# Kernel optimization log

Measured on AMD Instinct MI355X. Metric: run time of the kernel, lower is better.

## Reference

```python
import jax, jax.numpy as jnp
import numpy as np

N_NODES = 50000
N_EDGES = 1600000
IN_DIM = 16
HID = 128
N_ITER = 3
EPS = 1e-8


def _rownorm(x):
    # x / (||x||_2 per row + 1e-8), matching torch.norm(p='fro', dim=1, keepdim=True)
    return x / (jnp.linalg.norm(x, axis=-1, keepdims=True) + EPS)


def setup_inputs() -> dict:
    key = jax.random.key(0)
    ks = jax.random.split(key, 16)
    s = 0.05  # small init scale for numerical sanity
    inp = {
        'feat': jax.random.normal(ks[0], (N_NODES, IN_DIM), dtype=jnp.float32),
        'src': jax.random.randint(ks[1], (N_EDGES,), 0, N_NODES, dtype=jnp.int32),
        'dst': jax.random.randint(ks[2], (N_EDGES,), 0, N_NODES, dtype=jnp.int32),
        'init_W0': jax.random.normal(ks[3], (IN_DIM, HID), dtype=jnp.float32) * s,
        'init_b0': jnp.zeros((HID,), dtype=jnp.float32),
        'init_W1': jax.random.normal(ks[4], (HID, HID), dtype=jnp.float32) * s,
        'init_b1': jnp.zeros((HID,), dtype=jnp.float32),
        'init_W2': jax.random.normal(ks[5], (HID, HID), dtype=jnp.float32) * s,
        'init_b2': jnp.zeros((HID,), dtype=jnp.float32),
        'node_W0': jax.random.normal(ks[6], (N_ITER, 3 * HID, HID), dtype=jnp.float32) * s,
        'node_b0': jnp.zeros((N_ITER, HID), dtype=jnp.float32),
        'node_W1': jax.random.normal(ks[7], (N_ITER, HID, HID), dtype=jnp.float32) * s,
        'node_b1': jnp.zeros((N_ITER, HID), dtype=jnp.float32),
        'node_W2': jax.random.normal(ks[8], (N_ITER, HID, HID), dtype=jnp.float32) * s,
        'node_b2': jnp.zeros((N_ITER, HID), dtype=jnp.float32),
    }
    return inp


def reference(feat, src, dst,
              init_W0, init_b0, init_W1, init_b1, init_W2, init_b2,
              node_W0, node_b0, node_W1, node_b1, node_W2, node_b2):
    n = feat.shape[0]

    # init_network: MLP (Linear+ReLU for hidden layers, linear output)
    h = jax.nn.relu(feat @ init_W0 + init_b0)
    h = jax.nn.relu(h @ init_W1 + init_b1)
    h = h @ init_W2 + init_b2  # [N, HID]

    # global representation: normalized sum over all nodes (single graph)
    gr = _rownorm(jnp.sum(h, axis=0, keepdims=True))  # [1, HID]

    # DGL update_all only updates nodes with >=1 incoming edge
    deg = jax.ops.segment_sum(jnp.ones_like(src, dtype=jnp.float32), dst,
                              num_segments=n)
    has_in = (deg > 0)[:, None]  # [N, 1]

    for i in range(node_W0.shape[0]):
        # copy_u + mailbox sum == gather src features, segment-sum by dst
        msg = jax.ops.segment_sum(h[src], dst, num_segments=n)  # [N, HID]
        inp = jnp.concatenate(
            [msg, h, jnp.broadcast_to(gr, (n, gr.shape[1]))], axis=1)  # [N, 3*HID]
        out = jax.nn.relu(inp @ node_W0[i] + node_b0[i])
        out = jax.nn.relu(out @ node_W1[i] + node_b1[i])
        out = out @ node_W2[i] + node_b2[i]
        out = _rownorm(out)
        h = jnp.where(has_in, out, h)
        gr = _rownorm(jnp.sum(h, axis=0, keepdims=True))

    return h
```

## Files before the change

kernel.cpp:

```cpp
#include <hip/hip_runtime.h>
#include <hip/hip_bf16.h>

#define HID 128
#define IN_DIM 16
#define LDST 136
#define NBSH 6
#define BPAD 16
#define SRCM 0x3ffffffu
#define CH 8192
#define NBMAX 1024
#define NDPW 4

typedef unsigned short u16;
typedef __attribute__((ext_vector_type(8))) short short8;
typedef __attribute__((ext_vector_type(4))) float f32x4;

__device__ __forceinline__ u16 f2b(float f) {
    unsigned u = __float_as_uint(f);
    return (u16)((u + 0x7FFF + ((u >> 16) & 1)) >> 16);
}


__global__ __launch_bounds__(256) void hist_k(const int* __restrict__ dst, int* __restrict__ bktcnt,
                                              int E, int nb) {
    __shared__ int hist[NBMAX];
    int tid = threadIdx.x;
    int base = blockIdx.x * CH;
    int cnt = E - base; if (cnt > CH) cnt = CH;
    for (int i = tid; i < nb; i += 256) hist[i] = 0;
    __syncthreads();
    for (int j = tid; j < cnt; j += 256) atomicAdd(&hist[dst[base + j] >> NBSH], 1);
    __syncthreads();
    for (int i = tid; i < nb; i += 256) {
        int c = hist[i];
        if (c > 0) atomicAdd(&bktcnt[i], c);
    }
}

__global__ __launch_bounds__(1024) void bscan_k(const int* __restrict__ bktcnt, int* __restrict__ bktbase,
                                                int* __restrict__ bcnt, int* __restrict__ row_ptr,
                                                int nb, int n, int E) {
    __shared__ int sbuf[1024];
    int t = threadIdx.x;
    int v = (t < nb) ? bktcnt[t] : 0;
    sbuf[t] = v;
    __syncthreads();
    for (int off = 1; off < 1024; off <<= 1) {
        int a = (t >= off) ? sbuf[t - off] : 0;
        __syncthreads();
        sbuf[t] += a;
        __syncthreads();
    }
    if (t < nb) {
        int excl = sbuf[t] - v;
        bktbase[t] = excl;
        bcnt[t * BPAD] = excl;
    }
    if (t == 0) { bktbase[nb] = E; row_ptr[n] = E; }
}

__global__ __launch_bounds__(256) void bin_k(const int* __restrict__ src, const int* __restrict__ dst,
                                             int* __restrict__ bcnt, unsigned* __restrict__ ebuf,
                                             int E, int nb) {
    __shared__ unsigned stage[CH];
    __shared__ u16 sbk[CH];
    __shared__ int hist[NBMAX];
    __shared__ int lofs[NBMAX];
    __shared__ int sbase[NBMAX];
    __shared__ int scan256[256];
    int tid = threadIdx.x;
    int base = blockIdx.x * CH;
    int cnt = E - base; if (cnt > CH) cnt = CH;

    for (int i = tid; i < nb; i += 256) hist[i] = 0;
    __syncthreads();
    for (int j = tid; j < cnt; j += 256) {
        int d = dst[base + j];
        atomicAdd(&hist[d >> NBSH], 1);
    }
    __syncthreads();
    int psum[4];
    int ts = 0;
#pragma unroll
    for (int q = 0; q < 4; q++) {
        int idx = tid * 4 + q;
        int hv = (idx < nb) ? hist[idx] : 0;
        psum[q] = ts;
        ts += hv;
    }
    scan256[tid] = ts;
    __syncthreads();
    for (int off = 1; off < 256; off <<= 1) {
        int a = (tid >= off) ? scan256[tid - off] : 0;
        __syncthreads();
        scan256[tid] += a;
        __syncthreads();
    }
    int tbase = (tid > 0) ? scan256[tid - 1] : 0;
#pragma unroll
    for (int q = 0; q < 4; q++) {
        int idx = tid * 4 + q;
        if (idx < nb) lofs[idx] = tbase + psum[q];
    }
    __syncthreads();
    for (int i = tid; i < nb; i += 256) {
        int c = hist[i];
        if (c > 0) {
            int g = atomicAdd(&bcnt[i * BPAD], c);
            sbase[i] = g - lofs[i];
        }
    }
    __syncthreads();
    for (int j = tid; j < cnt; j += 256) {
        int e = base + j;
        int d = dst[e];
        int b = d >> NBSH;
        int r = atomicAdd(&lofs[b], 1);
        stage[r] = (unsigned)src[e] | ((unsigned)(d & 63) << 26);
        sbk[r] = (u16)b;
    }
    __syncthreads();
    for (int s = tid; s < cnt; s += 256) {
        int b = sbk[s];
        ebuf[sbase[b] + s] = stage[s];
    }
}

__global__ __launch_bounds__(256) void fill2_k(const unsigned* __restrict__ ebuf, const int* __restrict__ bktbase,
                                               int* __restrict__ row_ptr, int* __restrict__ deg,
                                               int* __restrict__ srcs, int n) {
    __shared__ int hist64[64];
    __shared__ int lofs[64];
    int tid = threadIdx.x;
    int b = blockIdx.x;
    int e0 = bktbase[b], e1 = bktbase[b + 1];
    if (tid < 64) hist64[tid] = 0;
    __syncthreads();
    for (int i = e0 + tid; i < e1; i += 256) atomicAdd(&hist64[ebuf[i] >> 26], 1);
    __syncthreads();
    if (tid < 64) {
        int d = hist64[tid];
        int s = d;
#pragma unroll
        for (int off = 1; off < 64; off <<= 1) {
            int t = __shfl_up(s, off);
            if (tid >= off) s += t;
        }
        int excl = e0 + s - d;
        int gi = (b << NBSH) + tid;
        if (gi < n) { row_ptr[gi] = excl; deg[gi] = d; }
        lofs[tid] = excl;
    }
    __syncthreads();
    for (int i = e0 + tid; i < e1; i += 256) {
        unsigned p = ebuf[i];
        int d = (int)(p >> 26);
        int pos = atomicAdd(&lofs[d], 1);
        srcs[pos] = (int)(p & SRCM);
    }
}


struct WJobs {
    const float* src[16];
    int dstoff[16];
    int ks[16];
};

__global__ __launch_bounds__(256) void wprep_k(WJobs j, u16* __restrict__ Wt,
                                               int* __restrict__ bktcnt, float* __restrict__ gsums,
                                               int nb, int gz) {
    int m = blockIdx.x;
    if (m == 0) {
        for (int i = threadIdx.x; i < nb; i += 256) bktcnt[i] = 0;
    } else if (m == 1) {
        for (int i = threadIdx.x; i < gz; i += 256) gsums[i] = 0.f;
    }
    const float* s = j.src[m];
    u16* d = Wt + j.dstoff[m];
    int ks = j.ks[m];
    if (ks == 8) {
        for (int idx = threadIdx.x; idx < 16384; idx += 256) {
            int jj = idx & 7;
            int lane = (idx >> 3) & 63;
            int ni = (idx >> 9) & 3;
            int kk = (idx >> 11) & 3;
            int half = idx >> 13;
            int k = kk * 32 + (lane >> 4) * 8 + jj;
            int col = half * 64 + ni * 16 + (lane & 15);
            d[idx] = f2b(s[k * HID + col]);
        }
        return;
    }
    int K = 1 << ks;
    int tot = K * HID;
    for (int idx = threadIdx.x; idx < tot; idx += 256) {
        int nn = idx >> ks;
        int kk = idx & (K - 1);
        d[idx] = f2b(s[kk * HID + nn]);
    }
}


__device__ __forceinline__ void unpack_add(uint4 v, float* a) {
    a[0] += __uint_as_float(v.x << 16);
    a[1] += __uint_as_float(v.x & 0xffff0000u);
    a[2] += __uint_as_float(v.y << 16);
    a[3] += __uint_as_float(v.y & 0xffff0000u);
    a[4] += __uint_as_float(v.z << 16);
    a[5] += __uint_as_float(v.z & 0xffff0000u);
    a[6] += __uint_as_float(v.w << 16);
    a[7] += __uint_as_float(v.w & 0xffff0000u);
}

__global__ __launch_bounds__(256) void msg_k(const u16* __restrict__ hb, const int* __restrict__ row_ptr,
                                             const int* __restrict__ srcs, u16* __restrict__ msgb, int n,
                                             const float* __restrict__ gsumIn, const float* __restrict__ Wg,
                                             const float* __restrict__ b0, float* __restrict__ grW) {
    if (blockIdx.x == gridDim.x - 1) {
        __shared__ float sred[2];
        __shared__ float sgr[HID];
        int t = threadIdx.x;
        if (t < HID) {
            float g = gsumIn[t];
            float s = g * g;
#pragma unroll
            for (int off = 1; off < 64; off <<= 1) s += __shfl_xor(s, off);
            if ((t & 63) == 0) sred[t >> 6] = s;
        }
        __syncthreads();
        if (t < HID) {
            float inv = 1.f / (sqrtf(sred[0] + sred[1]) + 1e-8f);
            sgr[t] = gsumIn[t] * inv;
        }
        __syncthreads();
        if (t < HID) {
            float a = b0[t];
#pragma unroll 4
            for (int k = 0; k < HID; k++) a += sgr[k] * Wg[k * HID + t];
            grW[t] = a;
        }
        return;
    }
    int wave = threadIdx.x >> 6, lane = threadIdx.x & 63;
    int g = lane >> 4;
    int l16 = lane & 15;
    int d0 = (blockIdx.x * 4 + wave) * NDPW;
    if (d0 >= n) return;
    int eNext = row_ptr[d0];
#pragma unroll 1
    for (int k = 0; k < NDPW; k++) {
        int d = d0 + k;
        if (d >= n) break;
        int e = eNext;
        int e1 = row_ptr[d + 1];
        eNext = e1;
        float a[8] = {0.f, 0.f, 0.f, 0.f, 0.f, 0.f, 0.f, 0.f};
        int s0 = 0, s1 = 0, s2 = 0, s3 = 0;
        if (e + 15 < e1) {
            s0 = srcs[e + g]; s1 = srcs[e + 4 + g];
            s2 = srcs[e + 8 + g]; s3 = srcs[e + 12 + g];
        }
        while (e + 15 < e1) {
            int t0 = s0, t1 = s1, t2 = s2, t3 = s3;
            int en = e + 16;
            if (en + 15 < e1) {
                s0 = srcs[en + g]; s1 = srcs[en + 4 + g];
                s2 = srcs[en + 8 + g]; s3 = srcs[en + 12 + g];
            }
            uint4 v0 = *(const uint4*)(hb + (size_t)t0 * HID + l16 * 8);
            uint4 v1 = *(const uint4*)(hb + (size_t)t1 * HID + l16 * 8);
            uint4 v2 = *(const uint4*)(hb + (size_t)t2 * HID + l16 * 8);
            uint4 v3 = *(const uint4*)(hb + (size_t)t3 * HID + l16 * 8);
            unpack_add(v0, a);
            unpack_add(v1, a);
            unpack_add(v2, a);
            unpack_add(v3, a);
            e = en;
        }
        if (e + 7 < e1) {
            int t0 = srcs[e + g], t1 = srcs[e + 4 + g];
            uint4 v0 = *(const uint4*)(hb + (size_t)t0 * HID + l16 * 8);
            uint4 v1 = *(const uint4*)(hb + (size_t)t1 * HID + l16 * 8);
            unpack_add(v0, a);
            unpack_add(v1, a);
            e += 8;
        }
        if (e + 3 < e1) {
            int s = srcs[e + g];
            uint4 v = *(const uint4*)(hb + (size_t)s * HID + l16 * 8);
            unpack_add(v, a);
            e += 4;
        }
        if (e + g < e1) {
            int s = srcs[e + g];
            uint4 v = *(const uint4*)(hb + (size_t)s * HID + l16 * 8);
            unpack_add(v, a);
        }
#pragma unroll
        for (int i = 0; i < 8; i++) {
            a[i] += __shfl_xor(a[i], 16);
            a[i] += __shfl_xor(a[i], 32);
        }
        if (g == 0) {
            uint4 o;
            o.x = (unsigned)f2b(a[0]) | ((unsigned)f2b(a[1]) << 16);
            o.y = (unsigned)f2b(a[2]) | ((unsigned)f2b(a[3]) << 16);
            o.z = (unsigned)f2b(a[4]) | ((unsigned)f2b(a[5]) << 16);
            o.w = (unsigned)f2b(a[6]) | ((unsigned)f2b(a[7]) << 16);
            *(uint4*)(msgb + (size_t)d * HID + l16 * 8) = o;
        }
    }
}


__device__ __forceinline__ void load_tile(const u16* __restrict__ base, int tid, uint4 p[4]) {
#pragma unroll
    for (int q = 0; q < 4; q++) {
        int c = tid + q * 512;
        p[q] = *(const uint4*)(base + (size_t)(c >> 4) * HID + (c & 15) * 8);
    }
}

__device__ __forceinline__ void write_tile(const uint4 p[4], int tid, u16* s) {
#pragma unroll
    for (int q = 0; q < 4; q++) {
        int c = tid + q * 512;
        *(uint4*)(s + (c >> 4) * LDST + (c & 15) * 8) = p[q];
    }
}

__device__ __forceinline__ void load_tile64(const u16* __restrict__ base, int tid, uint4 p[4]) {
#pragma unroll
    for (int q = 0; q < 4; q++) {
        int c = tid + q * 256;
        p[q] = *(const uint4*)(base + (size_t)(c >> 4) * HID + (c & 15) * 8);
    }
}

__device__ __forceinline__ void write_tile64(const uint4 p[4], int tid, u16* s) {
#pragma unroll
    for (int q = 0; q < 4; q++) {
        int c = tid + q * 256;
        *(uint4*)(s + (c >> 4) * LDST + (c & 15) * 8) = p[q];
    }
}

__device__ __forceinline__ void stageFeat(const float* __restrict__ feat, int row0, int n, int tid, u16* sA) {
    int row = tid >> 2, coff = tid & 3;
    ushort4 o = make_ushort4(0, 0, 0, 0);
    if (row0 + row < n) {
        float4 v = *(const float4*)(feat + (size_t)(row0 + row) * IN_DIM + coff * 4);
        o = make_ushort4(f2b(v.x), f2b(v.y), f2b(v.z), f2b(v.w));
    }
    *(ushort4*)(sA + row * LDST + coff * 4) = o;
    *(ushort4*)(sA + row * LDST + 16 + coff * 4) = make_ushort4(0, 0, 0, 0);
}

__device__ __forceinline__ void stageW16(const u16* __restrict__ Wt, int tid, u16* sB) {
    if (tid < 256) {
        int row = tid >> 1, h8 = tid & 1;
        uint4 v = *(const uint4*)(Wt + row * IN_DIM + h8 * 8);
        *(uint4*)(sB + row * LDST + h8 * 8) = v;
        *(uint4*)(sB + row * LDST + 16 + h8 * 8) = make_uint4(0, 0, 0, 0);
    }
}

template <int KSTEPS>
__device__ __forceinline__ void mac(const u16* sA, const u16* sB, int wrow, int wcol,
                                    int ln15, int quad, f32x4 acc[2][4]) {
#pragma unroll
    for (int kk = 0; kk < KSTEPS; kk++) {
        short8 a[2], b[4];
#pragma unroll
        for (int mi = 0; mi < 2; mi++)
            a[mi] = *(const short8*)(sA + (wrow + mi * 16 + ln15) * LDST + kk * 32 + quad * 8);
#pragma unroll
        for (int ni = 0; ni < 4; ni++)
            b[ni] = *(const short8*)(sB + (wcol + ni * 16 + ln15) * LDST + kk * 32 + quad * 8);
#pragma unroll
        for (int mi = 0; mi < 2; mi++)
#pragma unroll
            for (int ni = 0; ni < 4; ni++)
                acc[mi][ni] = __builtin_amdgcn_mfma_f32_16x16x32_bf16(a[mi], b[ni], acc[mi][ni], 0, 0, 0);
    }
}

__device__ __forceinline__ void macF(const u16* sA, const u16* __restrict__ Wf, int wrow, int half,
                                     int lane, int ln15, int quad, f32x4 acc[2][4]) {
    const u16* wb = Wf + (size_t)half * 8192;
#pragma unroll
    for (int kk = 0; kk < 4; kk++) {
        short8 a[2], b[4];
#pragma unroll
        for (int mi = 0; mi < 2; mi++)
            a[mi] = *(const short8*)(sA + (wrow + mi * 16 + ln15) * LDST + kk * 32 + quad * 8);
#pragma unroll
        for (int ni = 0; ni < 4; ni++)
            b[ni] = *(const short8*)(wb + (size_t)(((kk * 4 + ni) * 64) + lane) * 8);
#pragma unroll
        for (int mi = 0; mi < 2; mi++)
#pragma unroll
            for (int ni = 0; ni < 4; ni++)
                acc[mi][ni] = __builtin_amdgcn_mfma_f32_16x16x32_bf16(a[mi], b[ni], acc[mi][ni], 0, 0, 0);
    }
}

__device__ __forceinline__ void set_bias(f32x4 acc[2][4], const float* bias, int wcol, int ln15) {
#pragma unroll
    for (int ni = 0; ni < 4; ni++) {
        float bv = bias[wcol + ni * 16 + ln15];
#pragma unroll
        for (int mi = 0; mi < 2; mi++) acc[mi][ni] = (f32x4){bv, bv, bv, bv};
    }
}

__device__ __forceinline__ void acc_to_sA(const f32x4 acc[2][4], u16* sA, int wrow, int wcol,
                                          int ln15, int quad) {
#pragma unroll
    for (int mi = 0; mi < 2; mi++)
#pragma unroll
        for (int r = 0; r < 4; r++) {
            int row = wrow + mi * 16 + quad * 4 + r;
#pragma unroll
            for (int ni = 0; ni < 4; ni++)
                sA[row * LDST + wcol + ni * 16 + ln15] = f2b(fmaxf(acc[mi][ni][r], 0.f));
        }
}


__global__ __launch_bounds__(512, 4) void init_fused_k(const float* __restrict__ feat,
                                                       const u16* __restrict__ W0t, const u16* __restrict__ W1t,
                                                       const u16* __restrict__ W2t,
                                                       const float* __restrict__ b0, const float* __restrict__ b1,
                                                       const float* __restrict__ b2,
                                                       float* __restrict__ h, u16* __restrict__ hb,
                                                       float* __restrict__ gsum0, int n) {
    __shared__ u16 sA[128 * LDST];
    __shared__ u16 sB[128 * LDST];
    int tid = threadIdx.x;
    int lane = tid & 63, wave = tid >> 6;
    int ln15 = lane & 15, quad = lane >> 4;
    int wrow = (wave >> 1) * 32, wcol = (wave & 1) * 64;
    int row0 = blockIdx.x * 128;
    f32x4 acc[2][4];
    uint4 pB[4];

    stageFeat(feat, row0, n, tid, sA);
    stageW16(W0t, tid, sB);
    load_tile(W1t, tid, pB);
    set_bias(acc, b0, wcol, ln15);
    __syncthreads();
    mac<1>(sA, sB, wrow, wcol, ln15, quad, acc);
    __syncthreads();
    acc_to_sA(acc, sA, wrow, wcol, ln15, quad);
    write_tile(pB, tid, sB);
    load_tile(W2t, tid, pB);
    set_bias(acc, b1, wcol, ln15);
    __syncthreads();
    mac<4>(sA, sB, wrow, wcol, ln15, quad, acc);
    __syncthreads();
    acc_to_sA(acc, sA, wrow, wcol, ln15, quad);
    write_tile(pB, tid, sB);
    set_bias(acc, b2, wcol, ln15);
    __syncthreads();
    mac<4>(sA, sB, wrow, wcol, ln15, quad, acc);

    float csum[4] = {0.f, 0.f, 0.f, 0.f};
#pragma unroll
    for (int mi = 0; mi < 2; mi++)
#pragma unroll
        for (int r = 0; r < 4; r++) {
            int row = row0 + wrow + mi * 16 + quad * 4 + r;
            if (row < n) {
#pragma unroll
                for (int ni = 0; ni < 4; ni++) {
                    float v = acc[mi][ni][r];
                    int col = wcol + ni * 16 + ln15;
                    h[(size_t)row * HID + col] = v;
                    hb[(size_t)row * HID + col] = f2b(v);
                    csum[ni] += v;
                }
            }
        }
    __syncthreads();
    float* s_cs = (float*)sA;
    if (tid < HID) s_cs[tid] = 0.f;
    __syncthreads();
#pragma unroll
    for (int ni = 0; ni < 4; ni++) {
        float p = csum[ni];
        p += __shfl_xor(p, 16);
        p += __shfl_xor(p, 32);
        if (quad == 0) atomicAdd(&s_cs[wcol + ni * 16 + ln15], p);
    }
    __syncthreads();
    if (tid < HID) atomicAdd(&gsum0[tid], s_cs[tid]);
}


template <bool FINAL>
__global__ __launch_bounds__(256, 4) void node_fused_k(const u16* __restrict__ msgb, const u16* __restrict__ hbin,
                                                       const u16* __restrict__ W0af, const u16* __restrict__ W0bf,
                                                       const u16* __restrict__ W1f, const u16* __restrict__ W2f,
                                                       const float* __restrict__ grW,
                                                       const float* __restrict__ b1, const float* __restrict__ b2,
                                                       const int* __restrict__ deg,
                                                       float* __restrict__ h, u16* __restrict__ hb,
                                                       float* __restrict__ gsumOut, int n) {
    __shared__ u16 sA[64 * LDST];
    int tid = threadIdx.x;
    int lane = tid & 63, wave = tid >> 6;
    int ln15 = lane & 15, quad = lane >> 4;
    int wrow = (wave >> 1) * 32, half = wave & 1, wcol = half * 64;
    int row0 = blockIdx.x * 64;
    f32x4 acc[2][4];

    {
        uint4 tM[4];
        load_tile64(msgb + (size_t)row0 * HID, tid, tM);
        write_tile64(tM, tid, sA);
    }
    uint4 tH[4];
    load_tile64(hbin + (size_t)row0 * HID, tid, tH);
    set_bias(acc, grW, wcol, ln15);
    __syncthreads();
    macF(sA, W0af, wrow, half, lane, ln15, quad, acc);
    __syncthreads();
    write_tile64(tH, tid, sA);
    __syncthreads();
    macF(sA, W0bf, wrow, half, lane, ln15, quad, acc);
    __syncthreads();
    acc_to_sA(acc, sA, wrow, wcol, ln15, quad);
    set_bias(acc, b1, wcol, ln15);
    __syncthreads();
    macF(sA, W1f, wrow, half, lane, ln15, quad, acc);
    __syncthreads();
    acc_to_sA(acc, sA, wrow, wcol, ln15, quad);
    set_bias(acc, b2, wcol, ln15);
    __syncthreads();
    macF(sA, W2f, wrow, half, lane, ln15, quad, acc);

    __syncthreads();
    float* s_rs = (float*)sA;
    float* s_cs = (float*)sA + 64;
    if (tid < 64) s_rs[tid] = 0.f;
    else if (tid < 192) s_cs[tid - 64] = 0.f;
    __syncthreads();
#pragma unroll
    for (int mi = 0; mi < 2; mi++)
#pragma unroll
        for (int r = 0; r < 4; r++) {
            float p = 0.f;
#pragma unroll
            for (int ni = 0; ni < 4; ni++) { float v = acc[mi][ni][r]; p += v * v; }
            p += __shfl_xor(p, 1); p += __shfl_xor(p, 2);
            p += __shfl_xor(p, 4); p += __shfl_xor(p, 8);
            if (ln15 == 0) atomicAdd(&s_rs[wrow + mi * 16 + quad * 4 + r], p);
        }
    __syncthreads();
    float csum[4] = {0.f, 0.f, 0.f, 0.f};
#pragma unroll
    for (int mi = 0; mi < 2; mi++)
#pragma unroll
        for (int r = 0; r < 4; r++) {
            int rl = wrow + mi * 16 + quad * 4 + r;
            int row = row0 + rl;
            if (row < n) {
                bool upd = deg[row] > 0;
                float inv = 1.f / (sqrtf(s_rs[rl]) + 1e-8f);
#pragma unroll
                for (int ni = 0; ni < 4; ni++) {
                    int col = wcol + ni * 16 + ln15;
                    if (FINAL) {
                        if (upd) h[(size_t)row * HID + col] = acc[mi][ni][r] * inv;
                    } else {
                        float v;
                        if (upd) {
                            v = acc[mi][ni][r] * inv;
                            hb[(size_t)row * HID + col] = f2b(v);
                        } else {
                            v = h[(size_t)row * HID + col];
                        }
                        csum[ni] += v;
                    }
                }
            }
        }
    if (!FINAL) {
#pragma unroll
        for (int ni = 0; ni < 4; ni++) {
            float p = csum[ni];
            p += __shfl_xor(p, 16);
            p += __shfl_xor(p, 32);
            if (quad == 0) atomicAdd(&s_cs[wcol + ni * 16 + ln15], p);
        }
        __syncthreads();
        if (tid < HID) atomicAdd(&gsumOut[tid], s_cs[tid]);
    }
}


static inline char* align_up(char* p, size_t a) {
    return (char*)(((uintptr_t)p + a - 1) & ~(uintptr_t)(a - 1));
}

extern "C" void kernel_launch(void* const* d_in, const int* in_sizes, int n_in,
                              void* d_out, int out_size, void* d_ws, size_t ws_size,
                              hipStream_t stream) {
    const float* feat = (const float*)d_in[0];
    const int* src = (const int*)d_in[1];
    const int* dst = (const int*)d_in[2];
    const float* iW0 = (const float*)d_in[3];
    const float* ib0 = (const float*)d_in[4];
    const float* iW1 = (const float*)d_in[5];
    const float* ib1 = (const float*)d_in[6];
    const float* iW2 = (const float*)d_in[7];
    const float* ib2 = (const float*)d_in[8];
    const float* nW0 = (const float*)d_in[9];
    const float* nb0 = (const float*)d_in[10];
    const float* nW1 = (const float*)d_in[11];
    const float* nb1 = (const float*)d_in[12];
    const float* nW2 = (const float*)d_in[13];
    const float* nb2 = (const float*)d_in[14];

    int N = in_sizes[0] / IN_DIM;
    int E = in_sizes[1];
    int n_iter = in_sizes[10] / HID;
    int NB = (N + (1 << NBSH) - 1) >> NBSH;
    float* h = (float*)d_out;

    char* w = (char*)d_ws;
    size_t big2 = (size_t)(N + 128) * HID * sizeof(u16);
    u16* hb   = (u16*)w; w += big2;
    u16* msgb = (u16*)w; w += big2;
    float* gsums = (float*)w; w += (size_t)(n_iter + 1) * HID * sizeof(float);
    float* grW = (float*)w; w += 1024;
    u16* Wt = (u16*)w; w += (size_t)(2048 + 2 * 16384 + n_iter * 4 * 16384) * sizeof(u16);
    w = align_up(w, 16);
    int* deg = (int*)w; w += (size_t)N * 4;  w = align_up(w, 16);
    int* row_ptr = (int*)w; w += (size_t)(N + 1) * 4;  w = align_up(w, 16);
    int* bktcnt = (int*)w; w += (size_t)NB * 4;  w = align_up(w, 16);
    int* bktbase = (int*)w; w += (size_t)(NB + 1) * 4;  w = align_up(w, 64);
    int* bcnt = (int*)w; w += (size_t)NB * BPAD * 4;  w = align_up(w, 16);
    int* srcs = (int*)w; w += (size_t)E * 4;  w = align_up(w, 16);
    unsigned* ebuf = (unsigned*)w; w += (size_t)E * 4;
    (void)ws_size; (void)n_in; (void)out_size;

    const int OFF_IW0 = 0;
    const int OFF_IW1 = 2048;
    const int OFF_IW2 = 2048 + 16384;
    const int OFF_IT = 2048 + 2 * 16384;

    WJobs jobs;
    int nj = 0;
    jobs.src[nj] = iW0; jobs.dstoff[nj] = OFF_IW0; jobs.ks[nj] = 4; nj++;
    jobs.src[nj] = iW1; jobs.dstoff[nj] = OFF_IW1; jobs.ks[nj] = 7; nj++;
    jobs.src[nj] = iW2; jobs.dstoff[nj] = OFF_IW2; jobs.ks[nj] = 7; nj++;
    for (int i = 0; i < n_iter && nj + 4 <= 16; i++) {
        int base = OFF_IT + i * 4 * 16384;
        jobs.src[nj] = nW0 + (size_t)i * 3 * HID * HID;               jobs.dstoff[nj] = base;             jobs.ks[nj] = 8; nj++;
        jobs.src[nj] = nW0 + (size_t)i * 3 * HID * HID + HID * HID;   jobs.dstoff[nj] = base + 16384;     jobs.ks[nj] = 8; nj++;
        jobs.src[nj] = nW1 + (size_t)i * HID * HID;                   jobs.dstoff[nj] = base + 2 * 16384; jobs.ks[nj] = 8; nj++;
        jobs.src[nj] = nW2 + (size_t)i * HID * HID;                   jobs.dstoff[nj] = base + 3 * 16384; jobs.ks[nj] = 8; nj++;
    }

    wprep_k<<<nj, 256, 0, stream>>>(jobs, Wt, bktcnt, gsums, NB, (n_iter + 1) * HID);

    int cg = (E + CH - 1) / CH;
    hist_k<<<cg, 256, 0, stream>>>(dst, bktcnt, E, NB);
    bscan_k<<<1, 1024, 0, stream>>>(bktcnt, bktbase, bcnt, row_ptr, NB, N, E);
    bin_k<<<cg, 256, 0, stream>>>(src, dst, bcnt, ebuf, E, NB);
    fill2_k<<<NB, 256, 0, stream>>>(ebuf, bktbase, row_ptr, deg, srcs, N);

    int gb = (N + 127) / 128;
    int gb2 = (N + 63) / 64;
    int dpb = 4 * NDPW;
    int rb = (N + dpb - 1) / dpb;
    init_fused_k<<<gb, 512, 0, stream>>>(feat, Wt + OFF_IW0, Wt + OFF_IW1, Wt + OFF_IW2,
                                         ib0, ib1, ib2, h, hb, gsums, N);

    for (int i = 0; i < n_iter; i++) {
        const u16* Wit = Wt + OFF_IT + (size_t)i * 4 * 16384;
        const float* Wg = nW0 + (size_t)i * 3 * HID * HID + 2 * HID * HID;
        msg_k<<<rb + 1, 256, 0, stream>>>(hb, row_ptr, srcs, msgb, N,
                                          gsums + (size_t)i * HID, Wg, nb0 + (size_t)i * HID, grW);
        if (i + 1 < n_iter) {
            node_fused_k<false><<<gb2, 256, 0, stream>>>(msgb, hb, Wit, Wit + 16384, Wit + 2 * 16384,
                                                         Wit + 3 * 16384, grW, nb1 + (size_t)i * HID,
                                                         nb2 + (size_t)i * HID, deg, h, hb,
                                                         gsums + (size_t)(i + 1) * HID, N);
        } else {
            node_fused_k<true><<<gb2, 256, 0, stream>>>(msgb, hb, Wit, Wit + 16384, Wit + 2 * 16384,
                                                        Wit + 3 * 16384, grW, nb1 + (size_t)i * HID,
                                                        nb2 + (size_t)i * HID, deg, h, hb,
                                                        nullptr, N);
        }
    }
}
```

Baseline: 440.8 us.

## Merge graph-build kernels with weight prep and init MLP via block-range dispatch

Merges the edge histogram into the weight-prep kernel and the CSR fill into the init-MLP kernel, with blocks dispatched by index range so independent work shares one launch. The init MLP now uses 64-row tiles and reads fragment-ordered weights straight from global memory (macF) instead of staging them through LDS. Buffer zeroing moves to hipMemsetAsync. The aim is fewer kernel launches and better overlap of the small preprocessing stages, at the cost of two extra memset operations and more repeated global weight reads in the init MLP.

Result: no change. 445.8 us (+1.1%).

```diff
diff --git a/kernel.cpp b/kernel.cpp
--- a/kernel.cpp
+++ b/kernel.cpp
@@ -20,22 +20,6 @@
     return (u16)((u + 0x7FFF + ((u >> 16) & 1)) >> 16);
 }
 
-
-__global__ __launch_bounds__(256) void hist_k(const int* __restrict__ dst, int* __restrict__ bktcnt,
-                                              int E, int nb) {
-    __shared__ int hist[NBMAX];
-    int tid = threadIdx.x;
-    int base = blockIdx.x * CH;
-    int cnt = E - base; if (cnt > CH) cnt = CH;
-    for (int i = tid; i < nb; i += 256) hist[i] = 0;
-    __syncthreads();
-    for (int j = tid; j < cnt; j += 256) atomicAdd(&hist[dst[base + j] >> NBSH], 1);
-    __syncthreads();
-    for (int i = tid; i < nb; i += 256) {
-        int c = hist[i];
-        if (c > 0) atomicAdd(&bktcnt[i], c);
-    }
-}
 
 __global__ __launch_bounds__(1024) void bscan_k(const int* __restrict__ bktcnt, int* __restrict__ bktbase,
                                                 int* __restrict__ bcnt, int* __restrict__ row_ptr,
@@ -126,40 +110,6 @@
     }
 }
 
-__global__ __launch_bounds__(256) void fill2_k(const unsigned* __restrict__ ebuf, const int* __restrict__ bktbase,
-                                               int* __restrict__ row_ptr, int* __restrict__ deg,
-                                               int* __restrict__ srcs, int n) {
-    __shared__ int hist64[64];
-    __shared__ int lofs[64];
-    int tid = threadIdx.x;
-    int b = blockIdx.x;
-    int e0 = bktbase[b], e1 = bktbase[b + 1];
-    if (tid < 64) hist64[tid] = 0;
-    __syncthreads();
-    for (int i = e0 + tid; i < e1; i += 256) atomicAdd(&hist64[ebuf[i] >> 26], 1);
-    __syncthreads();
-    if (tid < 64) {
-        int d = hist64[tid];
-        int s = d;
-#pragma unroll
-        for (int off = 1; off < 64; off <<= 1) {
-            int t = __shfl_up(s, off);
-            if (tid >= off) s += t;
-        }
-        int excl = e0 + s - d;
-        int gi = (b << NBSH) + tid;
-        if (gi < n) { row_ptr[gi] = excl; deg[gi] = d; }
-        lofs[tid] = excl;
-    }
-    __syncthreads();
-    for (int i = e0 + tid; i < e1; i += 256) {
-        unsigned p = ebuf[i];
-        int d = (int)(p >> 26);
-        int pos = atomicAdd(&lofs[d], 1);
-        srcs[pos] = (int)(p & SRCM);
-    }
-}
-
 
 struct WJobs {
     const float* src[16];
@@ -167,20 +117,39 @@
     int ks[16];
 };
 
-__global__ __launch_bounds__(256) void wprep_k(WJobs j, u16* __restrict__ Wt,
-                                               int* __restrict__ bktcnt, float* __restrict__ gsums,
-                                               int nb, int gz) {
+__global__ __launch_bounds__(256) void preph_k(WJobs j, u16* __restrict__ Wt,
+                                               const int* __restrict__ dst, int* __restrict__ bktcnt,
+                                               int E, int nb, int nj) {
+    __shared__ int hist[NBMAX];
+    int tid = threadIdx.x;
+    if ((int)blockIdx.x >= nj) {
+        int base = (blockIdx.x - nj) * CH;
+        int cnt = E - base; if (cnt > CH) cnt = CH;
+        for (int i = tid; i < nb; i += 256) hist[i] = 0;
+        __syncthreads();
+        for (int jx = tid; jx < cnt; jx += 256) atomicAdd(&hist[dst[base + jx] >> NBSH], 1);
+        __syncthreads();
+        for (int i = tid; i < nb; i += 256) {
+            int c = hist[i];
+            if (c > 0) atomicAdd(&bktcnt[i], c);
+        }
+        return;
+    }
     int m = blockIdx.x;
-    if (m == 0) {
-        for (int i = threadIdx.x; i < nb; i += 256) bktcnt[i] = 0;
-    } else if (m == 1) {
-        for (int i = threadIdx.x; i < gz; i += 256) gsums[i] = 0.f;
-    }
     const float* s = j.src[m];
     u16* d = Wt + j.dstoff[m];
-    int ks = j.ks[m];
-    if (ks == 8) {
-        for (int idx = threadIdx.x; idx < 16384; idx += 256) {
+    if (j.ks[m] == 5) {
+        for (int idx = tid; idx < 4096; idx += 256) {
+            int jj = idx & 7;
+            int lane = (idx >> 3) & 63;
+            int ni = (idx >> 9) & 3;
+            int half = (idx >> 11) & 1;
+            int k = ((lane >> 4) << 3) + jj;
+            int col = half * 64 + ni * 16 + (lane & 15);
+            d[idx] = (k < IN_DIM) ? f2b(s[k * HID + col]) : (u16)0;
+        }
+    } else {
+        for (int idx = tid; idx < 16384; idx += 256) {
             int jj = idx & 7;
             int lane = (idx >> 3) & 63;
             int ni = (idx >> 9) & 3;
@@ -190,14 +159,6 @@
             int col = half * 64 + ni * 16 + (lane & 15);
             d[idx] = f2b(s[k * HID + col]);
         }
-        return;
-    }
-    int K = 1 << ks;
-    int tot = K * HID;
-    for (int idx = threadIdx.x; idx < tot; idx += 256) {
-        int nn = idx >> ks;
-        int kk = idx & (K - 1);
-        d[idx] = f2b(s[kk * HID + nn]);
     }
 }
 
@@ -314,22 +275,6 @@
 }
 
 
-__device__ __forceinline__ void load_tile(const u16* __restrict__ base, int tid, uint4 p[4]) {
-#pragma unroll
-    for (int q = 0; q < 4; q++) {
-        int c = tid + q * 512;
-        p[q] = *(const uint4*)(base + (size_t)(c >> 4) * HID + (c & 15) * 8);
-    }
-}
-
-__device__ __forceinline__ void write_tile(const uint4 p[4], int tid, u16* s) {
-#pragma unroll
-    for (int q = 0; q < 4; q++) {
-        int c = tid + q * 512;
-        *(uint4*)(s + (c >> 4) * LDST + (c & 15) * 8) = p[q];
-    }
-}
-
 __device__ __forceinline__ void load_tile64(const u16* __restrict__ base, int tid, uint4 p[4]) {
 #pragma unroll
     for (int q = 0; q < 4; q++) {
@@ -346,46 +291,6 @@
     }
 }
 
-__device__ __forceinline__ void stageFeat(const float* __restrict__ feat, int row0, int n, int tid, u16* sA) {
-    int row = tid >> 2, coff = tid & 3;
-    ushort4 o = make_ushort4(0, 0, 0, 0);
-    if (row0 + row < n) {
-        float4 v = *(const float4*)(feat + (size_t)(row0 + row) * IN_DIM + coff * 4);
-        o = make_ushort4(f2b(v.x), f2b(v.y), f2b(v.z), f2b(v.w));
-    }
-    *(ushort4*)(sA + row * LDST + coff * 4) = o;
-    *(ushort4*)(sA + row * LDST + 16 + coff * 4) = make_ushort4(0, 0, 0, 0);
-}
-
-__device__ __forceinline__ void stageW16(const u16* __restrict__ Wt, int tid, u16* sB) {
-    if (tid < 256) {
-        int row = tid >> 1, h8 = tid & 1;
-        uint4 v = *(const uint4*)(Wt + row * IN_DIM + h8 * 8);
-        *(uint4*)(sB + row * LDST + h8 * 8) = v;
-        *(uint4*)(sB + row * LDST + 16 + h8 * 8) = make_uint4(0, 0, 0, 0);
-    }
-}
-
-template <int KSTEPS>
-__device__ __forceinline__ void mac(const u16* sA, const u16* sB, int wrow, int wcol,
-                                    int ln15, int quad, f32x4 acc[2][4]) {
-#pragma unroll
-    for (int kk = 0; kk < KSTEPS; kk++) {
-        short8 a[2], b[4];
-#pragma unroll
-        for (int mi = 0; mi < 2; mi++)
-            a[mi] = *(const short8*)(sA + (wrow + mi * 16 + ln15) * LDST + kk * 32 + quad * 8);
-#pragma unroll
-        for (int ni = 0; ni < 4; ni++)
-            b[ni] = *(const short8*)(sB + (wcol + ni * 16 + ln15) * LDST + kk * 32 + quad * 8);
-#pragma unroll
-        for (int mi = 0; mi < 2; mi++)
-#pragma unroll
-            for (int ni = 0; ni < 4; ni++)
-                acc[mi][ni] = __builtin_amdgcn_mfma_f32_16x16x32_bf16(a[mi], b[ni], acc[mi][ni], 0, 0, 0);
-    }
-}
-
 __device__ __forceinline__ void macF(const u16* sA, const u16* __restrict__ Wf, int wrow, int half,
                                      int lane, int ln15, int quad, f32x4 acc[2][4]) {
     const u16* wb = Wf + (size_t)half * 8192;
@@ -429,42 +334,91 @@
 }
 
 
-__global__ __launch_bounds__(512, 4) void init_fused_k(const float* __restrict__ feat,
-                                                       const u16* __restrict__ W0t, const u16* __restrict__ W1t,
-                                                       const u16* __restrict__ W2t,
-                                                       const float* __restrict__ b0, const float* __restrict__ b1,
-                                                       const float* __restrict__ b2,
-                                                       float* __restrict__ h, u16* __restrict__ hb,
-                                                       float* __restrict__ gsum0, int n) {
-    __shared__ u16 sA[128 * LDST];
-    __shared__ u16 sB[128 * LDST];
+__global__ __launch_bounds__(256) void f2init_k(const unsigned* __restrict__ ebuf, const int* __restrict__ bktbase,
+                                                int* __restrict__ row_ptr, int* __restrict__ deg,
+                                                int* __restrict__ srcs,
+                                                const float* __restrict__ feat,
+                                                const u16* __restrict__ W0f, const u16* __restrict__ W1f,
+                                                const u16* __restrict__ W2f,
+                                                const float* __restrict__ b0, const float* __restrict__ b1,
+                                                const float* __restrict__ b2,
+                                                float* __restrict__ h, u16* __restrict__ hb,
+                                                float* __restrict__ gsum0, int n, int nbk) {
+    __shared__ u16 sA[64 * LDST];
     int tid = threadIdx.x;
+    if ((int)blockIdx.x < nbk) {
+        int* hist64 = (int*)sA;
+        int* lofs = (int*)sA + 64;
+        int b = blockIdx.x;
+        int e0 = bktbase[b], e1 = bktbase[b + 1];
+        if (tid < 64) hist64[tid] = 0;
+        __syncthreads();
+        for (int i = e0 + tid; i < e1; i += 256) atomicAdd(&hist64[ebuf[i] >> 26], 1);
+        __syncthreads();
+        if (tid < 64) {
+            int d = hist64[tid];
+            int s = d;
+#pragma unroll
+            for (int off = 1; off < 64; off <<= 1) {
+                int t = __shfl_up(s, off);
+                if (tid >= off) s += t;
+            }
+            int excl = e0 + s - d;
+            int gi = (b << NBSH) + tid;
+            if (gi < n) { row_ptr[gi] = excl; deg[gi] = d; }
+            lofs[tid] = excl;
+        }
+        __syncthreads();
+        for (int i = e0 + tid; i < e1; i += 256) {
+            unsigned p = ebuf[i];
+            int d = (int)(p >> 26);
+            int pos = atomicAdd(&lofs[d], 1);
+            srcs[pos] = (int)(p & SRCM);
+        }
+        return;
+    }
     int lane = tid & 63, wave = tid >> 6;
     int ln15 = lane & 15, quad = lane >> 4;
-    int wrow = (wave >> 1) * 32, wcol = (wave & 1) * 64;
-    int row0 = blockIdx.x * 128;
+    int wrow = (wave >> 1) * 32, half = wave & 1, wcol = half * 64;
+    int row0 = (blockIdx.x - nbk) * 64;
     f32x4 acc[2][4];
-    uint4 pB[4];
-
-    stageFeat(feat, row0, n, tid, sA);
-    stageW16(W0t, tid, sB);
-    load_tile(W1t, tid, pB);
+
+    {
+        int row = tid >> 2, coff = tid & 3;
+        ushort4 o = make_ushort4(0, 0, 0, 0);
+        if (row0 + row < n) {
+            float4 v = *(const float4*)(feat + (size_t)(row0 + row) * IN_DIM + coff * 4);
+            o = make_ushort4(f2b(v.x), f2b(v.y), f2b(v.z), f2b(v.w));
+        }
+        *(ushort4*)(sA + row * LDST + coff * 4) = o;
+        *(ushort4*)(sA + row * LDST + 16 + coff * 4) = make_ushort4(0, 0, 0, 0);
+    }
     set_bias(acc, b0, wcol, ln15);
     __syncthreads();
-    mac<1>(sA, sB, wrow, wcol, ln15, quad, acc);
+    {
+        short8 a[2], b[4];
+#pragma unroll
+        for (int mi = 0; mi < 2; mi++)
+            a[mi] = *(const short8*)(sA + (wrow + mi * 16 + ln15) * LDST + quad * 8);
+#pragma unroll
+        for (int ni = 0; ni < 4; ni++)
+            b[ni] = *(const short8*)(W0f + (size_t)((half * 4 + ni) * 64 + lane) * 8);
+#pragma unroll
+        for (int mi = 0; mi < 2; mi++)
+#pragma unroll
+            for (int ni = 0; ni < 4; ni++)
+                acc[mi][ni] = __builtin_amdgcn_mfma_f32_16x16x32_bf16(a[mi], b[ni], acc[mi][ni], 0, 0, 0);
+    }
     __syncthreads();
     acc_to_sA(acc, sA, wrow, wcol, ln15, quad);
-    write_tile(pB, tid, sB);
-    load_tile(W2t, tid, pB);
     set_bias(acc, b1, wcol, ln15);
     __syncthreads();
-    mac<4>(sA, sB, wrow, wcol, ln15, quad, acc);
+    macF(sA, W1f, wrow, half, lane, ln15, quad, acc);
     __syncthreads();
     acc_to_sA(acc, sA, wrow, wcol, ln15, quad);
-    write_tile(pB, tid, sB);
     set_bias(acc, b2, wcol, ln15);
     __syncthreads();
-    mac<4>(sA, sB, wrow, wcol, ln15, quad, acc);
+    macF(sA, W2f, wrow, half, lane, ln15, quad, acc);
 
     float csum[4] = {0.f, 0.f, 0.f, 0.f};
 #pragma unroll
@@ -636,7 +590,7 @@
     u16* msgb = (u16*)w; w += big2;
     float* gsums = (float*)w; w += (size_t)(n_iter + 1) * HID * sizeof(float);
     float* grW = (float*)w; w += 1024;
-    u16* Wt = (u16*)w; w += (size_t)(2048 + 2 * 16384 + n_iter * 4 * 16384) * sizeof(u16);
+    u16* Wt = (u16*)w; w += (size_t)(4096 + 2 * 16384 + n_iter * 4 * 16384) * sizeof(u16);
     w = align_up(w, 16);
     int* deg = (int*)w; w += (size_t)N * 4;  w = align_up(w, 16);
     int* row_ptr = (int*)w; w += (size_t)(N + 1) * 4;  w = align_up(w, 16);
@@ -648,15 +602,15 @@
     (void)ws_size; (void)n_in; (void)out_size;
 
     const int OFF_IW0 = 0;
-    const int OFF_IW1 = 2048;
-    const int OFF_IW2 = 2048 + 16384;
-    const int OFF_IT = 2048 + 2 * 16384;
+    const int OFF_IW1 = 4096;
+    const int OFF_IW2 = 4096 + 16384;
+    const int OFF_IT = 4096 + 2 * 16384;
 
     WJobs jobs;
     int nj = 0;
-    jobs.src[nj] = iW0; jobs.dstoff[nj] = OFF_IW0; jobs.ks[nj] = 4; nj++;
-    jobs.src[nj] = iW1; jobs.dstoff[nj] = OFF_IW1; jobs.ks[nj] = 7; nj++;
-    jobs.src[nj] = iW2; jobs.dstoff[nj] = OFF_IW2; jobs.ks[nj] = 7; nj++;
+    jobs.src[nj] = iW0; jobs.dstoff[nj] = OFF_IW0; jobs.ks[nj] = 5; nj++;
+    jobs.src[nj] = iW1; jobs.dstoff[nj] = OFF_IW1; jobs.ks[nj] = 8; nj++;
+    jobs.src[nj] = iW2; jobs.dstoff[nj] = OFF_IW2; jobs.ks[nj] = 8; nj++;
     for (int i = 0; i < n_iter && nj + 4 <= 16; i++) {
         int base = OFF_IT + i * 4 * 16384;
         jobs.src[nj] = nW0 + (size_t)i * 3 * HID * HID;               jobs.dstoff[nj] = base;             jobs.ks[nj] = 8; nj++;
@@ -665,21 +619,22 @@
         jobs.src[nj] = nW2 + (size_t)i * HID * HID;                   jobs.dstoff[nj] = base + 3 * 16384; jobs.ks[nj] = 8; nj++;
     }
 
-    wprep_k<<<nj, 256, 0, stream>>>(jobs, Wt, bktcnt, gsums, NB, (n_iter + 1) * HID);
+    hipMemsetAsync(bktcnt, 0, (size_t)NB * 4, stream);
+    hipMemsetAsync(gsums, 0, (size_t)(n_iter + 1) * HID * sizeof(float), stream);
 
     int cg = (E + CH - 1) / CH;
-    hist_k<<<cg, 256, 0, stream>>>(dst, bktcnt, E, NB);
+    preph_k<<<nj + cg, 256, 0, stream>>>(jobs, Wt, dst, bktcnt, E, NB, nj);
     bscan_k<<<1, 1024, 0, stream>>>(bktcnt, bktbase, bcnt, row_ptr, NB, N, E);
     bin_k<<<cg, 256, 0, stream>>>(src, dst, bcnt, ebuf, E, NB);
-    fill2_k<<<NB, 256, 0, stream>>>(ebuf, bktbase, row_ptr, deg, srcs, N);
-
-    int gb = (N + 127) / 128;
+
+    int gbi = (N + 63) / 64;
+    f2init_k<<<NB + gbi, 256, 0, stream>>>(ebuf, bktbase, row_ptr, deg, srcs,
+                                           feat, Wt + OFF_IW0, Wt + OFF_IW1, Wt + OFF_IW2,
+                                           ib0, ib1, ib2, h, hb, gsums, N, NB);
+
     int gb2 = (N + 63) / 64;
     int dpb = 4 * NDPW;
     int rb = (N + dpb - 1) / dpb;
-    init_fused_k<<<gb, 512, 0, stream>>>(feat, Wt + OFF_IW0, Wt + OFF_IW1, Wt + OFF_IW2,
-                                         ib0, ib1, ib2, h, hb, gsums, N);
-
     for (int i = 0; i < n_iter; i++) {
         const u16* Wit = Wt + OFF_IT + (size_t)i * 4 * 16384;
         const float* Wg = nW0 + (size_t)i * 3 * HID * HID + 2 * HID * HID;
```
